# Kernel tuning notes

Hardware: AMD Instinct MI355X
Metric: run time of the kernel (lower is better)

## Reference

```python
import jax, jax.numpy as jnp
import numpy as np

N, C, H, W = 64, 512, 16, 16
MEM_DIM, NUM_CLS = 2000, 10


def setup_inputs() -> dict:
    key = jax.random.key(0)
    k1, k2, k3 = jax.random.split(key, 3)
    z = jax.random.normal(k1, (N, C, H, W), dtype=jnp.float32)
    cls = jax.random.randint(k2, (N,), 0, NUM_CLS, dtype=jnp.int32)
    # nn.init.normal_(memory, 0.0, 0.02)
    memory = 0.02 * jax.random.normal(k3, (1, C, MEM_DIM, NUM_CLS), dtype=jnp.float32)
    return {"z": z, "cls": cls, "memory": memory}


def reference(z, cls, memory):
    n, c, h, w_ = z.shape
    hw = h * w_
    # memory[0,:,:,cls] -> (C, M, N) -> per-sample class memory (N, C, M)
    mem_cls = jnp.transpose(memory[0][:, :, cls], (2, 0, 1))  # (N, C, M)
    zf = z.reshape(n, c, hw)  # (N, C, HW)
    # similarity = -||z - m||^2 = 2 z.m - ||z||^2 - ||m||^2
    zm = jnp.einsum('ncp,ncm->npm', zf, mem_cls)          # (N, HW, M)
    z2 = jnp.sum(zf * zf, axis=1)[:, :, None]             # (N, HW, 1)
    m2 = jnp.sum(mem_cls * mem_cls, axis=1)[:, None, :]   # (N, 1, M)
    sim = 2.0 * zm - z2 - m2                               # (N, HW, M)
    log_w = jax.nn.log_softmax(sim, axis=2)
    w = jax.nn.softmax(sim, axis=2)
    w_hat = w  # topk == -1 in forward path
    # z_hat = bmm(mem_cls (N,C,M), w_hat^T (N,M,HW)) -> (N,C,HW)
    z_hat = jnp.einsum('ncm,npm->ncp', mem_cls, w_hat).reshape(n, c, h, w_)
    return (z_hat, w_hat, w, log_w)
```

## Files before the change

### kernel.cpp

```cpp
#include <hip/hip_runtime.h>
#include <hip/hip_bf16.h>
#include <math.h>

#define N_   64
#define C_   512
#define HW_  256
#define M_   2000
#define KCLS 10
#define MP_  2048
#define SIMS 4000

typedef __attribute__((ext_vector_type(8))) short bf16x8;
typedef __attribute__((ext_vector_type(4))) float f32x4;

__device__ __forceinline__ short f2bf(float x) {
    __hip_bfloat16 b = __float2bfloat16(x);
    return *reinterpret_cast<short*>(&b);
}
__device__ __forceinline__ float bf2f(short s) {
    __hip_bfloat16 b = *reinterpret_cast<__hip_bfloat16*>(&s);
    return __bfloat162float(b);
}

#define GATHER_LDS (KCLS * 32 * 66 * 2)
#define PART_LDS   (KCLS * 8 * 32 * 4)

__global__ __launch_bounds__(256) void prep_kernel(const float* __restrict__ mem,
                                                   const float* __restrict__ z,
                                                   const int* __restrict__ cls,
                                                   short* __restrict__ mcm,
                                                   short* __restrict__ mmc,
                                                   short* __restrict__ zTb,
                                                   float* __restrict__ m2,
                                                   int* __restrict__ perm) {
    __shared__ __align__(16) char smem[GATHER_LDS + PART_LDS];
    const int t = threadIdx.x;
    const int bid = blockIdx.x;

    if (bid < 512) {
        short (*tile)[32][66] = reinterpret_cast<short(*)[32][66]>(smem);
        float (*part)[8][32]  = reinterpret_cast<float(*)[8][32]>(smem + GATHER_LDS);
        const int m0 = (bid & 63) * 32;
        const int c0 = (bid >> 6) * 64;
        const int mm = t & 31;
        const int m = m0 + mm;
        const int cbase = t >> 5;
        float msum[KCLS];
#pragma unroll
        for (int k = 0; k < KCLS; ++k) msum[k] = 0.f;
        for (int ci = 0; ci < 8; ++ci) {
            const int cl = cbase + ci * 8;
            const int c = c0 + cl;
            short v[KCLS];
            if (m < M_) {
                const float* src = mem + ((size_t)c * M_ + m) * KCLS;
#pragma unroll
                for (int k = 0; k < KCLS; ++k) v[k] = f2bf(src[k]);
            } else {
#pragma unroll
                for (int k = 0; k < KCLS; ++k) v[k] = 0;
            }
#pragma unroll
            for (int k = 0; k < KCLS; ++k) {
                mcm[(size_t)k * (C_ * MP_) + (size_t)c * MP_ + m] = v[k];
                tile[k][mm][cl] = v[k];
                const float f = bf2f(v[k]);
                msum[k] = fmaf(f, f, msum[k]);
            }
        }
#pragma unroll
        for (int k = 0; k < KCLS; ++k) part[k][cbase][mm] = msum[k];
        __syncthreads();
        for (int idx = t; idx < KCLS * 32; idx += 256) {
            const int k = idx >> 5, mr = idx & 31;
            float s = 0.f;
#pragma unroll
            for (int cb = 0; cb < 8; ++cb) s += part[k][cb][mr];
            atomicAdd(&m2[k * MP_ + m0 + mr], s);
        }
        const int cc = t & 63;
        const int rbase = t >> 6;
        for (int k = 0; k < KCLS; ++k) {
#pragma unroll
            for (int r = 0; r < 8; ++r) {
                const int mm2 = r * 4 + rbase;
                mmc[(size_t)k * (MP_ * C_) + (size_t)(m0 + mm2) * C_ + c0 + cc] =
                    tile[k][mm2][cc];
            }
        }
    } else if (bid < 2560) {
        short (*tile)[70] = reinterpret_cast<short(*)[70]>(smem);
        const int b = bid - 512;
        const int c0 = (b & 7) * 64;
        const int p0 = ((b >> 3) & 3) * 64;
        const int n = b >> 5;
        const float* zp = z + (size_t)n * C_ * HW_;
        const int pp = t & 63;
        const int cb = t >> 6;
#pragma unroll
        for (int i = 0; i < 16; ++i) {
            const int cl = i * 4 + cb;
            tile[cl][pp] = f2bf(zp[(size_t)(c0 + cl) * HW_ + p0 + pp]);
        }
        __syncthreads();
        short* dst = zTb + (size_t)n * HW_ * C_;
        const int cc = t & 63;
        const int pb = t >> 6;
#pragma unroll
        for (int i = 0; i < 16; ++i) {
            const int pl = i * 4 + pb;
            dst[(size_t)(p0 + pl) * C_ + c0 + cc] = tile[cc][pl];
        }
    } else {
        int* lcls = reinterpret_cast<int*>(smem);
        if (t < N_) lcls[t] = cls[t];
        __syncthreads();
        if (t == 0) {
            int cnt[KCLS], pos[KCLS];
#pragma unroll
            for (int k = 0; k < KCLS; ++k) cnt[k] = 0;
            for (int n = 0; n < N_; ++n) cnt[lcls[n]]++;
            int acc = 0;
#pragma unroll
            for (int k = 0; k < KCLS; ++k) { pos[k] = acc; acc += cnt[k]; }
            for (int n = 0; n < N_; ++n) perm[pos[lcls[n]]++] = n;
        }
    }
}

template<int MODE>
__global__ __launch_bounds__(256) void gemm_nt(const short* __restrict__ Ab,
                                               const short* __restrict__ Bb,
                                               const float* __restrict__ Bf,
                                               const int* __restrict__ cls,
                                               const int* __restrict__ perm,
                                               const float* __restrict__ m2,
                                               float* __restrict__ Db) {
    constexpr int K  = (MODE == 0) ? C_ : MP_;
    constexpr int SA = (MODE == 0) ? C_ : MP_;
    constexpr int SB = (MODE == 0) ? C_ : MP_;
    constexpr int GX = (MODE == 0) ? 16 : 2;
    constexpr int GY = (MODE == 0) ? 2 : 4;
    constexpr int NWG = GX * GY * N_;
    constexpr int CPX = NWG / 8;

    const int flat = blockIdx.x + GX * (blockIdx.y + GY * blockIdx.z);
    const int logical = (flat & 7) * CPX + (flat >> 3);
    const int nl = logical / (GX * GY);
    const int n  = perm[nl];
    const int rr = logical % (GX * GY);
    const int by = rr / GX, bx = rr % GX;

    const int kc = cls[n];
    const int rowA0 = by * 128, colB0 = bx * 128;

    const short* A;
    const short* B  = nullptr;
    const float* BF = nullptr;
    if constexpr (MODE == 0) {
        A = Ab + (size_t)n * HW_ * C_;
        B = Bb + (size_t)kc * MP_ * C_;
    } else if constexpr (MODE == 1) {
        A = Ab + (size_t)kc * C_ * MP_;
        BF = Bf + (size_t)n * HW_ * M_;
    } else {
        A = Ab + (size_t)kc * C_ * MP_;
        B = Bb + (size_t)n * HW_ * MP_;
    }

    __shared__ short smem[2 * 128 * 64];
    short* As = smem;
    short* Bs = smem + 128 * 64;

    const int tid = threadIdx.x;
    const int w = tid >> 6, lane = tid & 63;
    const int wr = w >> 1, wc = w & 1;
    const int srow = lane >> 3, sslot = lane & 7;

    f32x4 acc[4][4];
#pragma unroll
    for (int i = 0; i < 4; ++i)
#pragma unroll
        for (int j = 0; j < 4; ++j) acc[i][j] = (f32x4){0.f, 0.f, 0.f, 0.f};

    for (int k0 = 0; k0 < K; k0 += 64) {
#pragma unroll
        for (int i = 0; i < 4; ++i) {
            const int row = w * 32 + i * 8 + srow;
            const int chunk = sslot ^ (row & 7);
            const short* src = A + (size_t)(rowA0 + row) * SA + k0 + chunk * 8;
            __builtin_amdgcn_global_load_lds(
                (const __attribute__((address_space(1))) void*)src,
                (__attribute__((address_space(3))) void*)&As[(w * 32 + i * 8) * 64],
                16, 0, 0);
        }
        if constexpr (MODE != 1) {
#pragma unroll
            for (int i = 0; i < 4; ++i) {
                const int row = w * 32 + i * 8 + srow;
                const int chunk = sslot ^ (row & 7);
                const short* src = B + (size_t)(colB0 + row) * SB + k0 + chunk * 8;
                __builtin_amdgcn_global_load_lds(
                    (const __attribute__((address_space(1))) void*)src,
                    (__attribute__((address_space(3))) void*)&Bs[(w * 32 + i * 8) * 64],
                    16, 0, 0);
            }
        } else {
#pragma unroll
            for (int i = 0; i < 4; ++i) {
                const int row = w * 32 + i * 8 + srow;
                const int kg = k0 + sslot * 8;
                float4 v0 = {0.f, 0.f, 0.f, 0.f}, v1 = {0.f, 0.f, 0.f, 0.f};
                if (kg < M_) {
                    const float* s = BF + (size_t)(colB0 + row) * M_ + kg;
                    v0 = *reinterpret_cast<const float4*>(s);
                    v1 = *reinterpret_cast<const float4*>(s + 4);
                }
                bf16x8 bv;
                bv[0] = f2bf(v0.x); bv[1] = f2bf(v0.y); bv[2] = f2bf(v0.z); bv[3] = f2bf(v0.w);
                bv[4] = f2bf(v1.x); bv[5] = f2bf(v1.y); bv[6] = f2bf(v1.z); bv[7] = f2bf(v1.w);
                *reinterpret_cast<bf16x8*>(&Bs[row * 64 + (sslot ^ (row & 7)) * 8]) = bv;
            }
        }
        __syncthreads();
        bf16x8 a[4][2], b[4][2];
#pragma unroll
        for (int i = 0; i < 4; ++i)
#pragma unroll
            for (int kk = 0; kk < 2; ++kk) {
                const int ra = wr * 64 + i * 16 + (lane & 15);
                const int slot = kk * 4 + (lane >> 4);
                a[i][kk] = *reinterpret_cast<const bf16x8*>(&As[ra * 64 + (slot ^ (ra & 7)) * 8]);
                const int rb = wc * 64 + i * 16 + (lane & 15);
                b[i][kk] = *reinterpret_cast<const bf16x8*>(&Bs[rb * 64 + (slot ^ (rb & 7)) * 8]);
            }
#pragma unroll
        for (int i = 0; i < 4; ++i)
#pragma unroll
            for (int j = 0; j < 4; ++j)
#pragma unroll
                for (int kk = 0; kk < 2; ++kk)
                    acc[i][j] = __builtin_amdgcn_mfma_f32_16x16x32_bf16(a[i][kk], b[j][kk], acc[i][j], 0, 0, 0);
        __syncthreads();
    }

    if constexpr (MODE == 0) {
        short* outs = smem;
#pragma unroll
        for (int i = 0; i < 4; ++i)
#pragma unroll
            for (int j = 0; j < 4; ++j) {
                const int col = wc * 64 + j * 16 + (lane & 15);
                const float m2v = m2[kc * MP_ + colB0 + col];
#pragma unroll
                for (int r = 0; r < 4; ++r) {
                    const int row = wr * 64 + i * 16 + (lane >> 4) * 4 + r;
                    outs[row * 128 + (col ^ (((row >> 2) & 7) << 3))] =
                        f2bf(2.f * acc[i][j][r] - m2v);
                }
            }
        __syncthreads();
        short* Ds = (short*)Db;
        const size_t rbase = (size_t)n * HW_ + rowA0;
#pragma unroll
        for (int it = 0; it < 8; ++it) {
            const int chunk = tid + it * 256;
            const int row = chunk >> 4, c8 = (chunk & 15) * 8;
            bf16x8 v = *reinterpret_cast<const bf16x8*>(
                &outs[row * 128 + (c8 ^ (((row >> 2) & 7) << 3))]);
            *reinterpret_cast<bf16x8*>(Ds + (rbase + row) * SIMS + colB0 + c8) = v;
        }
    } else {
        float* outf = (float*)smem;
        float* D = Db + (size_t)n * C_ * HW_;
#pragma unroll
        for (int h = 0; h < 2; ++h) {
            if (wr == h) {
#pragma unroll
                for (int i = 0; i < 4; ++i)
#pragma unroll
                    for (int j = 0; j < 4; ++j) {
                        const int col = wc * 64 + j * 16 + (lane & 15);
#pragma unroll
                        for (int r = 0; r < 4; ++r) {
                            const int row = i * 16 + (lane >> 4) * 4 + r;
                            outf[row * 128 + (col ^ (((row >> 2) & 1) << 4))] = acc[i][j][r];
                        }
                    }
            }
            __syncthreads();
#pragma unroll
            for (int it = 0; it < 8; ++it) {
                const int chunk = tid + it * 256;
                const int row = chunk >> 5, c4 = (chunk & 31) * 4;
                float4 v = *reinterpret_cast<const float4*>(
                    &outf[row * 128 + (c4 ^ (((row >> 2) & 1) << 4))]);
                *reinterpret_cast<float4*>(
                    &D[(size_t)(rowA0 + h * 64 + row) * HW_ + colB0 + c4]) = v;
            }
            __syncthreads();
        }
    }
}

__global__ __launch_bounds__(256) void softmax_kernel(const short* __restrict__ simb,
                                                      float* __restrict__ w_hat,
                                                      float* __restrict__ w,
                                                      float* __restrict__ logw,
                                                      short* __restrict__ wb,
                                                      int write_hat) {
    const int r = blockIdx.x;
    const int t = threadIdx.x;
    const bool valid = t < (M_ / 8);

    float s[8];
    if (valid) {
        bf16x8 v = *reinterpret_cast<const bf16x8*>(simb + (size_t)r * SIMS + t * 8);
#pragma unroll
        for (int i = 0; i < 8; ++i) s[i] = bf2f(v[i]);
    } else {
#pragma unroll
        for (int i = 0; i < 8; ++i) s[i] = -INFINITY;
    }

    float lmax = s[0];
#pragma unroll
    for (int i = 1; i < 8; ++i) lmax = fmaxf(lmax, s[i]);
#pragma unroll
    for (int off = 32; off >= 1; off >>= 1)
        lmax = fmaxf(lmax, __shfl_xor(lmax, off));

    __shared__ float wred[4];
    __shared__ float wsum[4];
    const int wid = t >> 6, lane = t & 63;
    if (lane == 0) wred[wid] = lmax;
    __syncthreads();
    const float gmax = fmaxf(fmaxf(wred[0], wred[1]), fmaxf(wred[2], wred[3]));

    float e[8];
    float lsum = 0.f;
    if (valid) {
#pragma unroll
        for (int i = 0; i < 8; ++i) {
            e[i] = __expf(s[i] - gmax);
            lsum += e[i];
        }
    }
#pragma unroll
    for (int off = 32; off >= 1; off >>= 1)
        lsum += __shfl_xor(lsum, off);
    if (lane == 0) wsum[wid] = lsum;
    __syncthreads();
    const float gsum = wsum[0] + wsum[1] + wsum[2] + wsum[3];
    const float inv = 1.f / gsum;
    const float lg  = __logf(gsum);

    if (valid) {
        const size_t base = (size_t)r * M_ + t * 8;
        float4 w0, w1, l0, l1;
        w0.x = e[0] * inv; w0.y = e[1] * inv; w0.z = e[2] * inv; w0.w = e[3] * inv;
        w1.x = e[4] * inv; w1.y = e[5] * inv; w1.z = e[6] * inv; w1.w = e[7] * inv;
        l0.x = s[0] - gmax - lg; l0.y = s[1] - gmax - lg;
        l0.z = s[2] - gmax - lg; l0.w = s[3] - gmax - lg;
        l1.x = s[4] - gmax - lg; l1.y = s[5] - gmax - lg;
        l1.z = s[6] - gmax - lg; l1.w = s[7] - gmax - lg;
        *reinterpret_cast<float4*>(w + base)     = w0;
        *reinterpret_cast<float4*>(w + base + 4) = w1;
        if (write_hat) {
            *reinterpret_cast<float4*>(w_hat + base)     = w0;
            *reinterpret_cast<float4*>(w_hat + base + 4) = w1;
        }
        *reinterpret_cast<float4*>(logw + base)     = l0;
        *reinterpret_cast<float4*>(logw + base + 4) = l1;
        if (wb) {
            bf16x8 bv;
            bv[0] = f2bf(w0.x); bv[1] = f2bf(w0.y); bv[2] = f2bf(w0.z); bv[3] = f2bf(w0.w);
            bv[4] = f2bf(w1.x); bv[5] = f2bf(w1.y); bv[6] = f2bf(w1.z); bv[7] = f2bf(w1.w);
            *reinterpret_cast<bf16x8*>(wb + (size_t)r * MP_ + t * 8) = bv;
        }
    } else if (wb) {
        bf16x8 zv = {0, 0, 0, 0, 0, 0, 0, 0};
        *reinterpret_cast<bf16x8*>(wb + (size_t)r * MP_ + t * 8) = zv;
    }
}

__global__ __launch_bounds__(256) void copy_kernel(const float* __restrict__ src,
                                                   float* __restrict__ dst, int n4) {
    int i = blockIdx.x * 256 + threadIdx.x;
    int stride = gridDim.x * 256;
    for (; i < n4; i += stride)
        reinterpret_cast<float4*>(dst)[i] = reinterpret_cast<const float4*>(src)[i];
}

extern "C" void kernel_launch(void* const* d_in, const int* in_sizes, int n_in,
                              void* d_out, int out_size, void* d_ws, size_t ws_size,
                              hipStream_t stream) {
    const float* z      = (const float*)d_in[0];
    const int*   cls    = (const int*)d_in[1];
    const float* memory = (const float*)d_in[2];

    float* out   = (float*)d_out;
    float* z_hat = out;
    float* w_hat = z_hat + (size_t)N_ * C_ * HW_;
    float* w     = w_hat + (size_t)N_ * HW_ * M_;
    float* logw  = w     + (size_t)N_ * HW_ * M_;

    const size_t mcm_sh = (size_t)KCLS * C_ * MP_;
    const size_t mmc_sh = mcm_sh;
    const size_t zTb_sh = (size_t)N_ * HW_ * C_;
    const size_t wb_sh  = (size_t)N_ * HW_ * MP_;
    const size_t m2_fl  = (size_t)KCLS * MP_;
    const size_t need_base = (mcm_sh + mmc_sh + zTb_sh) * 2 + m2_fl * 4 + 256;
    const size_t need_full = need_base + wb_sh * 2;

    short *mcm, *mmc, *zTb, *wb = nullptr;
    float* m2;
    int* perm;
    int write_hat;
    if (ws_size >= need_base) {
        char* p = (char*)d_ws;
        mcm  = (short*)p;         p += mcm_sh * 2;
        mmc  = (short*)p;         p += mmc_sh * 2;
        m2   = (float*)p;         p += m2_fl * 4;
        perm = (int*)p;           p += 256;
        zTb  = (short*)p;         p += zTb_sh * 2;
        if (ws_size >= need_full) wb = (short*)p;
        write_hat = 1;
    } else {
        char* p = (char*)w_hat;
        mcm  = (short*)p;         p += mcm_sh * 2;
        mmc  = (short*)p;         p += mmc_sh * 2;
        m2   = (float*)p;         p += m2_fl * 4;
        perm = (int*)p;
        zTb  = (short*)z_hat;
        write_hat = 0;
    }
    short* simb = (short*)logw;

    hipMemsetAsync(m2, 0, m2_fl * sizeof(float), stream);
    prep_kernel<<<2561, 256, 0, stream>>>(memory, z, cls, mcm, mmc, zTb, m2, perm);
    gemm_nt<0><<<dim3(16, 2, N_), 256, 0, stream>>>(zTb, mmc, nullptr, cls, perm, m2, logw);
    softmax_kernel<<<N_ * HW_, 256, 0, stream>>>(simb, w_hat, w, logw, wb, write_hat);
    if (wb)
        gemm_nt<2><<<dim3(2, 4, N_), 256, 0, stream>>>(mcm, wb, nullptr, cls, perm, m2, z_hat);
    else
        gemm_nt<1><<<dim3(2, 4, N_), 256, 0, stream>>>(mcm, nullptr, w, cls, perm, m2, z_hat);
    if (!write_hat)
        copy_kernel<<<2048, 256, 0, stream>>>(w, w_hat, (N_ * HW_ * M_) / 4);
}
```

Before: 263.0 us.

## Fuse similarity GEMM with unnormalized softmax exp and defer normalization to z_hat GEMM

Replaces the sim GEMM plus separate softmax kernel with one kernel that computes each 32-row strip's similarities, applies exp directly without max subtraction (clamped at 60), stores bf16 unnormalized probabilities and row sums, and then writes w, w_hat and log_w. The z_hat GEMM consumes the unnormalized probabilities and scales by 1/rowsum in its epilogue. This drops the bf16 sim round-trip and a whole kernel launch. In exchange it relies on the similarity values never overflowing, it derives log_w from log of bf16 exp values (losing precision and underflowing to -inf for very negative sims), and it runs only 512 smaller blocks, which may lower GEMM efficiency.

```diff
diff --git a/kernel.cpp b/kernel.cpp
--- a/kernel.cpp
+++ b/kernel.cpp
@@ -128,45 +128,187 @@
     }
 }
 
-template<int MODE>
-__global__ __launch_bounds__(256) void gemm_nt(const short* __restrict__ Ab,
-                                               const short* __restrict__ Bb,
-                                               const float* __restrict__ Bf,
-                                               const int* __restrict__ cls,
-                                               const int* __restrict__ perm,
-                                               const float* __restrict__ m2,
-                                               float* __restrict__ Db) {
-    constexpr int K  = (MODE == 0) ? C_ : MP_;
-    constexpr int SA = (MODE == 0) ? C_ : MP_;
-    constexpr int SB = (MODE == 0) ? C_ : MP_;
-    constexpr int GX = (MODE == 0) ? 16 : 2;
-    constexpr int GY = (MODE == 0) ? 2 : 4;
-    constexpr int NWG = GX * GY * N_;
-    constexpr int CPX = NWG / 8;
-
-    const int flat = blockIdx.x + GX * (blockIdx.y + GY * blockIdx.z);
-    const int logical = (flat & 7) * CPX + (flat >> 3);
-    const int nl = logical / (GX * GY);
-    const int n  = perm[nl];
-    const int rr = logical % (GX * GY);
-    const int by = rr / GX, bx = rr % GX;
-
+template<int MERGED>
+__global__ __launch_bounds__(256) void simsm_kernel(
+    const short* __restrict__ zTb, const short* __restrict__ mmc,
+    const int* __restrict__ cls, const int* __restrict__ perm,
+    const float* __restrict__ m2, short* __restrict__ P, const int pstride,
+    float* __restrict__ rowsum, float* __restrict__ w_hat,
+    float* __restrict__ w, float* __restrict__ logw)
+{
+    __shared__ short As[32 * 512];
+    __shared__ short Bs[128 * 128];
+    __shared__ short Ps[32 * 128];
+    __shared__ float rpart[32][4];
+    __shared__ float inv_l[32], lg_l[32];
+
+    const int flat = blockIdx.x;
+    const int logical = (flat & 7) * 64 + (flat >> 3);
+    const int nl = logical >> 3;
+    const int pt = logical & 7;
+    const int n = perm[nl];
     const int kc = cls[n];
-    const int rowA0 = by * 128, colB0 = bx * 128;
-
-    const short* A;
-    const short* B  = nullptr;
-    const float* BF = nullptr;
-    if constexpr (MODE == 0) {
-        A = Ab + (size_t)n * HW_ * C_;
-        B = Bb + (size_t)kc * MP_ * C_;
-    } else if constexpr (MODE == 1) {
-        A = Ab + (size_t)kc * C_ * MP_;
-        BF = Bf + (size_t)n * HW_ * M_;
-    } else {
-        A = Ab + (size_t)kc * C_ * MP_;
-        B = Bb + (size_t)n * HW_ * MP_;
-    }
+    const int p0 = pt * 32;
+
+    const short* A = zTb + (size_t)n * HW_ * C_;
+    const short* B = mmc + (size_t)kc * MP_ * C_;
+    short* myP = P + (size_t)(n * HW_ + p0) * pstride;
+
+    const int tid = threadIdx.x;
+    const int wv = tid >> 6, lane = tid & 63;
+    const int lo = lane & 15, hi = lane >> 4;
+
+#pragma unroll
+    for (int i = 0; i < 8; ++i) {
+        const int row = i * 4 + wv;
+        const short* src = A + (size_t)(p0 + row) * C_ + ((lane ^ (row & 7)) << 3);
+        __builtin_amdgcn_global_load_lds(
+            (const __attribute__((address_space(1))) void*)src,
+            (__attribute__((address_space(3))) void*)&As[row * 512],
+            16, 0, 0);
+    }
+
+    float rsum[2][4];
+#pragma unroll
+    for (int i = 0; i < 2; ++i)
+#pragma unroll
+        for (int r = 0; r < 4; ++r) rsum[i][r] = 0.f;
+
+    for (int mc = 0; mc < 16; ++mc) {
+        f32x4 acc[2][2];
+#pragma unroll
+        for (int i = 0; i < 2; ++i)
+#pragma unroll
+            for (int j = 0; j < 2; ++j) acc[i][j] = (f32x4){0.f, 0.f, 0.f, 0.f};
+
+        for (int ks = 0; ks < 4; ++ks) {
+#pragma unroll
+            for (int i = 0; i < 8; ++i) {
+                const int row = i * 16 + wv * 4 + hi;
+                const int chunk = lo ^ (row & 7);
+                const short* src = B + (size_t)(mc * 128 + row) * C_ + ks * 128 + (chunk << 3);
+                __builtin_amdgcn_global_load_lds(
+                    (const __attribute__((address_space(1))) void*)src,
+                    (__attribute__((address_space(3))) void*)&Bs[(i * 16 + wv * 4) * 128],
+                    16, 0, 0);
+            }
+            __syncthreads();
+            bf16x8 a[2][4], b[2][4];
+#pragma unroll
+            for (int i = 0; i < 2; ++i)
+#pragma unroll
+                for (int kk = 0; kk < 4; ++kk) {
+                    const int ra = i * 16 + lo;
+                    const int sa = ks * 16 + kk * 4 + hi;
+                    a[i][kk] = *reinterpret_cast<const bf16x8*>(
+                        &As[ra * 512 + ((sa ^ (ra & 7)) << 3)]);
+                    const int rb = wv * 32 + i * 16 + lo;
+                    const int sb = kk * 4 + hi;
+                    b[i][kk] = *reinterpret_cast<const bf16x8*>(
+                        &Bs[rb * 128 + ((sb ^ (rb & 7)) << 3)]);
+                }
+#pragma unroll
+            for (int i = 0; i < 2; ++i)
+#pragma unroll
+                for (int j = 0; j < 2; ++j)
+#pragma unroll
+                    for (int kk = 0; kk < 4; ++kk)
+                        acc[i][j] = __builtin_amdgcn_mfma_f32_16x16x32_bf16(
+                            a[i][kk], b[j][kk], acc[i][j], 0, 0, 0);
+            __syncthreads();
+        }
+
+#pragma unroll
+        for (int i = 0; i < 2; ++i)
+#pragma unroll
+            for (int j = 0; j < 2; ++j) {
+                const int colL = wv * 32 + j * 16 + lo;
+                const int mg = mc * 128 + colL;
+                const float m2v = m2[kc * MP_ + mg];
+#pragma unroll
+                for (int r = 0; r < 4; ++r) {
+                    const int row = i * 16 + hi * 4 + r;
+                    const float s = 2.f * acc[i][j][r] - m2v;
+                    const float pv = (mg < M_) ? __expf(fminf(s, 60.f)) : 0.f;
+                    rsum[i][r] += pv;
+                    Ps[row * 128 + (colL ^ ((row & 7) << 3))] = f2bf(pv);
+                }
+            }
+        __syncthreads();
+#pragma unroll
+        for (int it = 0; it < 2; ++it) {
+            const int cc = tid + it * 256;
+            const int prow = cc >> 4, g = cc & 15;
+            bf16x8 v = *reinterpret_cast<const bf16x8*>(
+                &Ps[prow * 128 + ((g ^ (prow & 7)) << 3)]);
+            *reinterpret_cast<bf16x8*>(myP + (size_t)prow * pstride + mc * 128 + (g << 3)) = v;
+        }
+    }
+
+#pragma unroll
+    for (int i = 0; i < 2; ++i)
+#pragma unroll
+        for (int r = 0; r < 4; ++r) {
+            float v = rsum[i][r];
+            v += __shfl_xor(v, 1); v += __shfl_xor(v, 2);
+            v += __shfl_xor(v, 4); v += __shfl_xor(v, 8);
+            if (lo == 0) rpart[i * 16 + hi * 4 + r][wv] = v;
+        }
+    __syncthreads();
+    if (tid < 32) {
+        const float s = rpart[tid][0] + rpart[tid][1] + rpart[tid][2] + rpart[tid][3];
+        rowsum[n * HW_ + p0 + tid] = s;
+        inv_l[tid] = 1.f / s;
+        lg_l[tid] = __logf(s);
+    }
+
+    if (MERGED) {
+        __threadfence();
+        __syncthreads();
+        for (int idx = tid; idx < 32 * (M_ / 8); idx += 256) {
+            const int row = idx / (M_ / 8);
+            const int m8 = (idx - row * (M_ / 8)) * 8;
+            bf16x8 pvv = *reinterpret_cast<const bf16x8*>(
+                myP + (size_t)row * pstride + m8);
+            const float inv = inv_l[row], lg = lg_l[row];
+            float pf[8];
+#pragma unroll
+            for (int q = 0; q < 8; ++q) pf[q] = bf2f(pvv[q]);
+            float4 w0, w1, l0, l1;
+            w0.x = pf[0] * inv; w0.y = pf[1] * inv; w0.z = pf[2] * inv; w0.w = pf[3] * inv;
+            w1.x = pf[4] * inv; w1.y = pf[5] * inv; w1.z = pf[6] * inv; w1.w = pf[7] * inv;
+            l0.x = __logf(pf[0]) - lg; l0.y = __logf(pf[1]) - lg;
+            l0.z = __logf(pf[2]) - lg; l0.w = __logf(pf[3]) - lg;
+            l1.x = __logf(pf[4]) - lg; l1.y = __logf(pf[5]) - lg;
+            l1.z = __logf(pf[6]) - lg; l1.w = __logf(pf[7]) - lg;
+            const size_t ob = (size_t)(n * HW_ + p0 + row) * M_ + m8;
+            *reinterpret_cast<float4*>(w + ob)         = w0;
+            *reinterpret_cast<float4*>(w + ob + 4)     = w1;
+            *reinterpret_cast<float4*>(w_hat + ob)     = w0;
+            *reinterpret_cast<float4*>(w_hat + ob + 4) = w1;
+            *reinterpret_cast<float4*>(logw + ob)      = l0;
+            *reinterpret_cast<float4*>(logw + ob + 4)  = l1;
+        }
+    }
+}
+
+__global__ __launch_bounds__(256) void zhat_kernel(
+    const short* __restrict__ mcm, const short* __restrict__ P, const int pstride,
+    const int* __restrict__ cls, const int* __restrict__ perm,
+    const float* __restrict__ rowsum, float* __restrict__ zhat)
+{
+    const int flat = blockIdx.x;
+    const int logical = (flat & 7) * 64 + (flat >> 3);
+    const int nl = logical >> 3;
+    const int rr = logical & 7;
+    const int n = perm[nl];
+    const int kc = cls[n];
+    const int ct = rr >> 1, ptb = rr & 1;
+    const int rowA0 = ct * 128, colB0 = ptb * 128;
+
+    const short* A = mcm + (size_t)kc * C_ * MP_;
+    const short* B = P + (size_t)n * HW_ * pstride;
+    float* D = zhat + (size_t)n * C_ * HW_;
 
     __shared__ short smem[2 * 128 * 64];
     short* As = smem;
@@ -183,44 +325,21 @@
 #pragma unroll
         for (int j = 0; j < 4; ++j) acc[i][j] = (f32x4){0.f, 0.f, 0.f, 0.f};
 
-    for (int k0 = 0; k0 < K; k0 += 64) {
+    for (int k0 = 0; k0 < MP_; k0 += 64) {
 #pragma unroll
         for (int i = 0; i < 4; ++i) {
             const int row = w * 32 + i * 8 + srow;
             const int chunk = sslot ^ (row & 7);
-            const short* src = A + (size_t)(rowA0 + row) * SA + k0 + chunk * 8;
+            const short* srcA = A + (size_t)(rowA0 + row) * MP_ + k0 + (chunk << 3);
             __builtin_amdgcn_global_load_lds(
-                (const __attribute__((address_space(1))) void*)src,
+                (const __attribute__((address_space(1))) void*)srcA,
                 (__attribute__((address_space(3))) void*)&As[(w * 32 + i * 8) * 64],
                 16, 0, 0);
-        }
-        if constexpr (MODE != 1) {
-#pragma unroll
-            for (int i = 0; i < 4; ++i) {
-                const int row = w * 32 + i * 8 + srow;
-                const int chunk = sslot ^ (row & 7);
-                const short* src = B + (size_t)(colB0 + row) * SB + k0 + chunk * 8;
-                __builtin_amdgcn_global_load_lds(
-                    (const __attribute__((address_space(1))) void*)src,
-                    (__attribute__((address_space(3))) void*)&Bs[(w * 32 + i * 8) * 64],
-                    16, 0, 0);
-            }
-        } else {
-#pragma unroll
-            for (int i = 0; i < 4; ++i) {
-                const int row = w * 32 + i * 8 + srow;
-                const int kg = k0 + sslot * 8;
-                float4 v0 = {0.f, 0.f, 0.f, 0.f}, v1 = {0.f, 0.f, 0.f, 0.f};
-                if (kg < M_) {
-                    const float* s = BF + (size_t)(colB0 + row) * M_ + kg;
-                    v0 = *reinterpret_cast<const float4*>(s);
-                    v1 = *reinterpret_cast<const float4*>(s + 4);
-                }
-                bf16x8 bv;
-                bv[0] = f2bf(v0.x); bv[1] = f2bf(v0.y); bv[2] = f2bf(v0.z); bv[3] = f2bf(v0.w);
-                bv[4] = f2bf(v1.x); bv[5] = f2bf(v1.y); bv[6] = f2bf(v1.z); bv[7] = f2bf(v1.w);
-                *reinterpret_cast<bf16x8*>(&Bs[row * 64 + (sslot ^ (row & 7)) * 8]) = bv;
-            }
+            const short* srcB = B + (size_t)(colB0 + row) * pstride + k0 + (chunk << 3);
+            __builtin_amdgcn_global_load_lds(
+                (const __attribute__((address_space(1))) void*)srcB,
+                (__attribute__((address_space(3))) void*)&Bs[(w * 32 + i * 8) * 64],
+                16, 0, 0);
         }
         __syncthreads();
         bf16x8 a[4][2], b[4][2];
@@ -230,9 +349,9 @@
             for (int kk = 0; kk < 2; ++kk) {
                 const int ra = wr * 64 + i * 16 + (lane & 15);
                 const int slot = kk * 4 + (lane >> 4);
-                a[i][kk] = *reinterpret_cast<const bf16x8*>(&As[ra * 64 + (slot ^ (ra & 7)) * 8]);
+                a[i][kk] = *reinterpret_cast<const bf16x8*>(&As[ra * 64 + ((slot ^ (ra & 7)) << 3)]);
                 const int rb = wc * 64 + i * 16 + (lane & 15);
-                b[i][kk] = *reinterpret_cast<const bf16x8*>(&Bs[rb * 64 + (slot ^ (rb & 7)) * 8]);
+                b[i][kk] = *reinterpret_cast<const bf16x8*>(&Bs[rb * 64 + ((slot ^ (rb & 7)) << 3)]);
             }
 #pragma unroll
         for (int i = 0; i < 4; ++i)
@@ -244,152 +363,78 @@
         __syncthreads();
     }
 
-    if constexpr (MODE == 0) {
-        short* outs = smem;
-#pragma unroll
-        for (int i = 0; i < 4; ++i)
-#pragma unroll
-            for (int j = 0; j < 4; ++j) {
-                const int col = wc * 64 + j * 16 + (lane & 15);
-                const float m2v = m2[kc * MP_ + colB0 + col];
-#pragma unroll
-                for (int r = 0; r < 4; ++r) {
-                    const int row = wr * 64 + i * 16 + (lane >> 4) * 4 + r;
-                    outs[row * 128 + (col ^ (((row >> 2) & 7) << 3))] =
-                        f2bf(2.f * acc[i][j][r] - m2v);
+    float alpha[4];
+#pragma unroll
+    for (int j = 0; j < 4; ++j)
+        alpha[j] = 1.f / rowsum[n * HW_ + colB0 + wc * 64 + j * 16 + (lane & 15)];
+
+    float* outf = (float*)smem;
+#pragma unroll
+    for (int h = 0; h < 2; ++h) {
+        if (wr == h) {
+#pragma unroll
+            for (int i = 0; i < 4; ++i)
+#pragma unroll
+                for (int j = 0; j < 4; ++j) {
+                    const int col = wc * 64 + j * 16 + (lane & 15);
+#pragma unroll
+                    for (int r = 0; r < 4; ++r) {
+                        const int row = i * 16 + (lane >> 4) * 4 + r;
+                        outf[row * 128 + (col ^ (((row >> 2) & 1) << 4))] = acc[i][j][r] * alpha[j];
+                    }
                 }
-            }
-        __syncthreads();
-        short* Ds = (short*)Db;
-        const size_t rbase = (size_t)n * HW_ + rowA0;
+        }
+        __syncthreads();
 #pragma unroll
         for (int it = 0; it < 8; ++it) {
             const int chunk = tid + it * 256;
-            const int row = chunk >> 4, c8 = (chunk & 15) * 8;
-            bf16x8 v = *reinterpret_cast<const bf16x8*>(
-                &outs[row * 128 + (c8 ^ (((row >> 2) & 7) << 3))]);
-            *reinterpret_cast<bf16x8*>(Ds + (rbase + row) * SIMS + colB0 + c8) = v;
-        }
-    } else {
-        float* outf = (float*)smem;
-        float* D = Db + (size_t)n * C_ * HW_;
-#pragma unroll
-        for (int h = 0; h < 2; ++h) {
-            if (wr == h) {
-#pragma unroll
-                for (int i = 0; i < 4; ++i)
-#pragma unroll
-                    for (int j = 0; j < 4; ++j) {
-                        const int col = wc * 64 + j * 16 + (lane & 15);
-#pragma unroll
-                        for (int r = 0; r < 4; ++r) {
-                            const int row = i * 16 + (lane >> 4) * 4 + r;
-                            outf[row * 128 + (col ^ (((row >> 2) & 1) << 4))] = acc[i][j][r];
-                        }
-                    }
-            }
-            __syncthreads();
-#pragma unroll
-            for (int it = 0; it < 8; ++it) {
-                const int chunk = tid + it * 256;
-                const int row = chunk >> 5, c4 = (chunk & 31) * 4;
-                float4 v = *reinterpret_cast<const float4*>(
-                    &outf[row * 128 + (c4 ^ (((row >> 2) & 1) << 4))]);
-                *reinterpret_cast<float4*>(
-                    &D[(size_t)(rowA0 + h * 64 + row) * HW_ + colB0 + c4]) = v;
-            }
-            __syncthreads();
-        }
-    }
-}
-
-__global__ __launch_bounds__(256) void softmax_kernel(const short* __restrict__ simb,
-                                                      float* __restrict__ w_hat,
-                                                      float* __restrict__ w,
-                                                      float* __restrict__ logw,
-                                                      short* __restrict__ wb,
-                                                      int write_hat) {
+            const int row = chunk >> 5, c4 = (chunk & 31) * 4;
+            float4 v = *reinterpret_cast<const float4*>(
+                &outf[row * 128 + (c4 ^ (((row >> 2) & 1) << 4))]);
+            *reinterpret_cast<float4*>(
+                &D[(size_t)(rowA0 + h * 64 + row) * HW_ + colB0 + c4]) = v;
+        }
+        __syncthreads();
+    }
+}
+
+__global__ __launch_bounds__(256) void finish_kernel(const short* __restrict__ P,
+                                                     const float* __restrict__ rowsum,
+                                                     float* __restrict__ w_hat,
+                                                     float* __restrict__ w,
+                                                     float* __restrict__ logw) {
     const int r = blockIdx.x;
     const int t = threadIdx.x;
     const bool valid = t < (M_ / 8);
-
-    float s[8];
+    float pf[8];
     if (valid) {
-        bf16x8 v = *reinterpret_cast<const bf16x8*>(simb + (size_t)r * SIMS + t * 8);
-#pragma unroll
-        for (int i = 0; i < 8; ++i) s[i] = bf2f(v[i]);
+        bf16x8 v = *reinterpret_cast<const bf16x8*>(P + (size_t)r * SIMS + t * 8);
+#pragma unroll
+        for (int q = 0; q < 8; ++q) pf[q] = bf2f(v[q]);
     } else {
 #pragma unroll
-        for (int i = 0; i < 8; ++i) s[i] = -INFINITY;
-    }
-
-    float lmax = s[0];
-#pragma unroll
-    for (int i = 1; i < 8; ++i) lmax = fmaxf(lmax, s[i]);
-#pragma unroll
-    for (int off = 32; off >= 1; off >>= 1)
-        lmax = fmaxf(lmax, __shfl_xor(lmax, off));
-
-    __shared__ float wred[4];
-    __shared__ float wsum[4];
-    const int wid = t >> 6, lane = t & 63;
-    if (lane == 0) wred[wid] = lmax;
+        for (int q = 0; q < 8; ++q) pf[q] = 1.f;
+    }
+    const float gsum = rowsum[r];
+    const float inv = 1.f / gsum;
+    const float lg = __logf(gsum);
     __syncthreads();
-    const float gmax = fmaxf(fmaxf(wred[0], wred[1]), fmaxf(wred[2], wred[3]));
-
-    float e[8];
-    float lsum = 0.f;
     if (valid) {
-#pragma unroll
-        for (int i = 0; i < 8; ++i) {
-            e[i] = __expf(s[i] - gmax);
-            lsum += e[i];
-        }
-    }
-#pragma unroll
-    for (int off = 32; off >= 1; off >>= 1)
-        lsum += __shfl_xor(lsum, off);
-    if (lane == 0) wsum[wid] = lsum;
-    __syncthreads();
-    const float gsum = wsum[0] + wsum[1] + wsum[2] + wsum[3];
-    const float inv = 1.f / gsum;
-    const float lg  = __logf(gsum);
-
-    if (valid) {
-        const size_t base = (size_t)r * M_ + t * 8;
+        const size_t ob = (size_t)r * M_ + t * 8;
         float4 w0, w1, l0, l1;
-        w0.x = e[0] * inv; w0.y = e[1] * inv; w0.z = e[2] * inv; w0.w = e[3] * inv;
-        w1.x = e[4] * inv; w1.y = e[5] * inv; w1.z = e[6] * inv; w1.w = e[7] * inv;
-        l0.x = s[0] - gmax - lg; l0.y = s[1] - gmax - lg;
-        l0.z = s[2] - gmax - lg; l0.w = s[3] - gmax - lg;
-        l1.x = s[4] - gmax - lg; l1.y = s[5] - gmax - lg;
-        l1.z = s[6] - gmax - lg; l1.w = s[7] - gmax - lg;
-        *reinterpret_cast<float4*>(w + base)     = w0;
-        *reinterpret_cast<float4*>(w + base + 4) = w1;
-        if (write_hat) {
-            *reinterpret_cast<float4*>(w_hat + base)     = w0;
-            *reinterpret_cast<float4*>(w_hat + base + 4) = w1;
-        }
-        *reinterpret_cast<float4*>(logw + base)     = l0;
-        *reinterpret_cast<float4*>(logw + base + 4) = l1;
-        if (wb) {
-            bf16x8 bv;
-            bv[0] = f2bf(w0.x); bv[1] = f2bf(w0.y); bv[2] = f2bf(w0.z); bv[3] = f2bf(w0.w);
-            bv[4] = f2bf(w1.x); bv[5] = f2bf(w1.y); bv[6] = f2bf(w1.z); bv[7] = f2bf(w1.w);
-            *reinterpret_cast<bf16x8*>(wb + (size_t)r * MP_ + t * 8) = bv;
-        }
-    } else if (wb) {
-        bf16x8 zv = {0, 0, 0, 0, 0, 0, 0, 0};
-        *reinterpret_cast<bf16x8*>(wb + (size_t)r * MP_ + t * 8) = zv;
-    }
-}
-
-__global__ __launch_bounds__(256) void copy_kernel(const float* __restrict__ src,
-                                                   float* __restrict__ dst, int n4) {
-    int i = blockIdx.x * 256 + threadIdx.x;
-    int stride = gridDim.x * 256;
-    for (; i < n4; i += stride)
-        reinterpret_cast<float4*>(dst)[i] = reinterpret_cast<const float4*>(src)[i];
+        w0.x = pf[0] * inv; w0.y = pf[1] * inv; w0.z = pf[2] * inv; w0.w = pf[3] * inv;
+        w1.x = pf[4] * inv; w1.y = pf[5] * inv; w1.z = pf[6] * inv; w1.w = pf[7] * inv;
+        l0.x = __logf(pf[0]) - lg; l0.y = __logf(pf[1]) - lg;
+        l0.z = __logf(pf[2]) - lg; l0.w = __logf(pf[3]) - lg;
+        l1.x = __logf(pf[4]) - lg; l1.y = __logf(pf[5]) - lg;
+        l1.z = __logf(pf[6]) - lg; l1.w = __logf(pf[7]) - lg;
+        *reinterpret_cast<float4*>(w + ob)         = w0;
+        *reinterpret_cast<float4*>(w + ob + 4)     = w1;
+        *reinterpret_cast<float4*>(w_hat + ob)     = w0;
+        *reinterpret_cast<float4*>(w_hat + ob + 4) = w1;
+        *reinterpret_cast<float4*>(logw + ob)      = l0;
+        *reinterpret_cast<float4*>(logw + ob + 4)  = l1;
+    }
 }
 
 extern "C" void kernel_launch(void* const* d_in, const int* in_sizes, int n_in,
@@ -408,43 +453,48 @@
     const size_t mcm_sh = (size_t)KCLS * C_ * MP_;
     const size_t mmc_sh = mcm_sh;
     const size_t zTb_sh = (size_t)N_ * HW_ * C_;
-    const size_t wb_sh  = (size_t)N_ * HW_ * MP_;
+    const size_t P_sh   = (size_t)N_ * HW_ * MP_;
     const size_t m2_fl  = (size_t)KCLS * MP_;
-    const size_t need_base = (mcm_sh + mmc_sh + zTb_sh) * 2 + m2_fl * 4 + 256;
-    const size_t need_full = need_base + wb_sh * 2;
-
-    short *mcm, *mmc, *zTb, *wb = nullptr;
-    float* m2;
+    const size_t rs_fl  = (size_t)N_ * HW_;
+    const size_t need_main = (mcm_sh + mmc_sh + zTb_sh + P_sh) * 2
+                           + (m2_fl + rs_fl) * 4 + 256;
+
+    short *mcm, *mmc, *zTb, *P;
+    float *m2, *rowsum;
     int* perm;
-    int write_hat;
-    if (ws_size >= need_base) {
+    int merged;
+    if (ws_size >= need_main) {
         char* p = (char*)d_ws;
-        mcm  = (short*)p;         p += mcm_sh * 2;
-        mmc  = (short*)p;         p += mmc_sh * 2;
-        m2   = (float*)p;         p += m2_fl * 4;
-        perm = (int*)p;           p += 256;
-        zTb  = (short*)p;         p += zTb_sh * 2;
-        if (ws_size >= need_full) wb = (short*)p;
-        write_hat = 1;
+        mcm    = (short*)p;  p += mcm_sh * 2;
+        mmc    = (short*)p;  p += mmc_sh * 2;
+        m2     = (float*)p;  p += m2_fl * 4;
+        rowsum = (float*)p;  p += rs_fl * 4;
+        perm   = (int*)p;    p += 256;
+        zTb    = (short*)p;  p += zTb_sh * 2;
+        P      = (short*)p;
+        merged = 1;
     } else {
         char* p = (char*)w_hat;
-        mcm  = (short*)p;         p += mcm_sh * 2;
-        mmc  = (short*)p;         p += mmc_sh * 2;
-        m2   = (float*)p;         p += m2_fl * 4;
-        perm = (int*)p;
-        zTb  = (short*)z_hat;
-        write_hat = 0;
-    }
-    short* simb = (short*)logw;
+        mcm    = (short*)p;  p += mcm_sh * 2;
+        mmc    = (short*)p;  p += mmc_sh * 2;
+        m2     = (float*)p;  p += m2_fl * 4;
+        rowsum = (float*)p;  p += rs_fl * 4;
+        perm   = (int*)p;
+        zTb    = (short*)z_hat;
+        P      = (short*)logw;
+        merged = 0;
+    }
 
     hipMemsetAsync(m2, 0, m2_fl * sizeof(float), stream);
     prep_kernel<<<2561, 256, 0, stream>>>(memory, z, cls, mcm, mmc, zTb, m2, perm);
-    gemm_nt<0><<<dim3(16, 2, N_), 256, 0, stream>>>(zTb, mmc, nullptr, cls, perm, m2, logw);
-    softmax_kernel<<<N_ * HW_, 256, 0, stream>>>(simb, w_hat, w, logw, wb, write_hat);
-    if (wb)
-        gemm_nt<2><<<dim3(2, 4, N_), 256, 0, stream>>>(mcm, wb, nullptr, cls, perm, m2, z_hat);
-    else
-        gemm_nt<1><<<dim3(2, 4, N_), 256, 0, stream>>>(mcm, nullptr, w, cls, perm, m2, z_hat);
-    if (!write_hat)
-        copy_kernel<<<2048, 256, 0, stream>>>(w, w_hat, (N_ * HW_ * M_) / 4);
-}
+    if (merged) {
+        simsm_kernel<1><<<512, 256, 0, stream>>>(zTb, mmc, cls, perm, m2, P, MP_,
+                                                 rowsum, w_hat, w, logw);
+        zhat_kernel<<<512, 256, 0, stream>>>(mcm, P, MP_, cls, perm, rowsum, z_hat);
+    } else {
+        simsm_kernel<0><<<512, 256, 0, stream>>>(zTb, mmc, cls, perm, m2, P, SIMS,
+                                                 rowsum, w_hat, w, logw);
+        zhat_kernel<<<512, 256, 0, stream>>>(mcm, P, SIMS, cls, perm, rowsum, z_hat);
+        finish_kernel<<<N_ * HW_, 256, 0, stream>>>(P, rowsum, w_hat, w, logw);
+    }
+}
```

After: 369.8 us. 40.6% more time.
